# Kernel optimization log

Hardware: AMD Instinct MI355X
Metric: run time of the kernel (lower is better)

Reference implementation:

```python
import jax, jax.numpy as jnp
import numpy as np

N_NODES = 50000   # nodes per channel
N_EDGES = 800000  # intra edges per channel (avg degree ~16)
N_GRAPHS = 64     # graphs in the batch (global_add_pool segments)
D = 128           # node_features_len == out_channels
L = 3             # n_layers
BN_EPS = 1e-5
NEG_SLOPE = 0.01  # F.leaky_relu default


def setup_inputs() -> dict:
    key = jax.random.key(0)
    ks = jax.random.split(key, 24)
    s = 0.05
    inp = {
        "x1": jax.random.normal(ks[0], (N_NODES, D), jnp.float32),
        "x2": jax.random.normal(ks[1], (N_NODES, D), jnp.float32),
        # GIN MLP channel 1: Linear-BN-ReLU-Linear-ReLU, stacked over layers
        "W1_ch1": jax.random.normal(ks[2], (L, D, D), jnp.float32) * s,
        "b1_ch1": jax.random.normal(ks[3], (L, D), jnp.float32) * s,
        "bn_g": 1.0 + jax.random.normal(ks[4], (L, D), jnp.float32) * s,
        "bn_b": jax.random.normal(ks[5], (L, D), jnp.float32) * s,
        "bn_m": jax.random.normal(ks[6], (L, D), jnp.float32) * s,
        "bn_v": 0.5 + jax.random.uniform(ks[7], (L, D), jnp.float32),
        "W2_ch1": jax.random.normal(ks[8], (L, D, D), jnp.float32) * s,
        "b2_ch1": jax.random.normal(ks[9], (L, D), jnp.float32) * s,
        # GIN MLP channel 2: Linear-ReLU-Linear
        "W1_ch2": jax.random.normal(ks[10], (L, D, D), jnp.float32) * s,
        "b1_ch2": jax.random.normal(ks[11], (L, D), jnp.float32) * s,
        "W2_ch2": jax.random.normal(ks[12], (L, D, D), jnp.float32) * s,
        "b2_ch2": jax.random.normal(ks[13], (L, D), jnp.float32) * s,
        # head: Linear(2*D*L -> D) - ReLU - Dropout - Linear(D -> 1)
        "Wf1": jax.random.normal(ks[14], (2 * D * L, D), jnp.float32) * s,
        "bf1": jax.random.normal(ks[15], (D,), jnp.float32) * s,
        "Wf2": jax.random.normal(ks[16], (D, 1), jnp.float32) * s,
        "bf2": jax.random.normal(ks[17], (1,), jnp.float32) * s,
        "edge1": jax.random.randint(ks[18], (2, N_EDGES), 0, N_NODES, dtype=jnp.int32),
        "edge2": jax.random.randint(ks[19], (2, N_EDGES), 0, N_NODES, dtype=jnp.int32),
        "batch1": jnp.sort(jax.random.randint(ks[20], (N_NODES,), 0, N_GRAPHS, dtype=jnp.int32)),
        "batch2": jnp.sort(jax.random.randint(ks[21], (N_NODES,), 0, N_GRAPHS, dtype=jnp.int32)),
    }
    return inp


def _aggregate(x, edge):
    # GINConv sum aggregation: message x[src] scattered to dst; eps=0 default
    return jax.ops.segment_sum(x[edge[0]], edge[1], num_segments=N_NODES)


def _channel1(x, edge, batch, W1, b1, g, b, m, v, W2, b2):
    pooled = []
    for i in range(L):
        h = (x + _aggregate(x, edge)) @ W1[i] + b1[i]
        h = (h - m[i]) * (g[i] / jnp.sqrt(v[i] + BN_EPS)) + b[i]  # eval-mode BN
        h = jax.nn.relu(h)
        h = jax.nn.relu(h @ W2[i] + b2[i])
        x = jax.nn.leaky_relu(h, NEG_SLOPE)
        pooled.append(jax.ops.segment_sum(x, batch, num_segments=N_GRAPHS))
    return jnp.concatenate(pooled, axis=-1)  # [G, D*L]


def _channel2(x, edge, batch, W1, b1, W2, b2):
    pooled = []
    for i in range(L):
        h = jax.nn.relu((x + _aggregate(x, edge)) @ W1[i] + b1[i])
        h = h @ W2[i] + b2[i]
        x = jax.nn.leaky_relu(h, NEG_SLOPE)
        pooled.append(jax.ops.segment_sum(x, batch, num_segments=N_GRAPHS))
    return jnp.concatenate(pooled, axis=-1)  # [G, D*L]


def reference(x1, x2, W1_ch1, b1_ch1, bn_g, bn_b, bn_m, bn_v, W2_ch1, b2_ch1,
              W1_ch2, b1_ch2, W2_ch2, b2_ch2, Wf1, bf1, Wf2, bf2,
              edge1, edge2, batch1, batch2):
    p1 = _channel1(x1, edge1, batch1, W1_ch1, b1_ch1, bn_g, bn_b, bn_m, bn_v, W2_ch1, b2_ch1)
    p2 = _channel2(x2, edge2, batch2, W1_ch2, b1_ch2, W2_ch2, b2_ch2)
    z = jnp.concatenate([p1, p2], axis=-1)  # [G, 2*D*L]
    h = jax.nn.relu(z @ Wf1 + bf1)          # dropout is identity in eval mode
    return h @ Wf2 + bf2                    # [G, 1]
```

## Files before the change

### kernel.cpp

```cpp
#include <hip/hip_runtime.h>

#define NN 50000
#define NE 800000
#define TOTN (2 * NN)
#define NG 64
#define DD 128
#define NL 3
#define ZW (2 * DD * NL)
#define NB2 128
#define NPB 391
#define CAP2 8192
#define CHUNK 4096
#define P1B 196
#define GB2 1024

typedef __attribute__((ext_vector_type(8))) short short8;
typedef __attribute__((ext_vector_type(4))) float f32x4;

__device__ inline unsigned short f2bf(float f) {
  unsigned int u = __float_as_uint(f);
  unsigned int r = (u + 0x7fffu + ((u >> 16) & 1u)) >> 16;
  return (unsigned short)r;
}
__device__ inline float bflo(unsigned int u) { return __uint_as_float(u << 16); }
__device__ inline float bfhi(unsigned int u) { return __uint_as_float(u & 0xffff0000u); }

__global__ __launch_bounds__(256) void cvt_x_kernel(const float* __restrict__ x1,
                                                    const float* __restrict__ x2,
                                                    unsigned short* __restrict__ X) {
  int i = blockIdx.x * 256 + threadIdx.x;
  if (i >= TOTN * DD / 8) return;
  const int per = NN * DD / 8;
  int ch = i >= per;
  const float* x = ch ? x2 : x1;
  int il = i - ch * per;
  const float4* in4 = reinterpret_cast<const float4*>(x);
  float4 a = in4[2 * il], b = in4[2 * il + 1];
  uint4 o;
  o.x = (unsigned int)f2bf(a.x) | ((unsigned int)f2bf(a.y) << 16);
  o.y = (unsigned int)f2bf(a.z) | ((unsigned int)f2bf(a.w) << 16);
  o.z = (unsigned int)f2bf(b.x) | ((unsigned int)f2bf(b.y) << 16);
  o.w = (unsigned int)f2bf(b.z) | ((unsigned int)f2bf(b.w) << 16);
  reinterpret_cast<uint4*>(X)[i] = o;
}

__global__ __launch_bounds__(256) void cvt_wt_kernel(const float* __restrict__ p0,
                                                     const float* __restrict__ p1,
                                                     const float* __restrict__ p2,
                                                     const float* __restrict__ p3,
                                                     unsigned short* __restrict__ out) {
  __shared__ float tile[32][33];
  int slot = blockIdx.z;
  int grp = slot / 3, mat = slot % 3;
  const float* ip = (grp == 0 ? p0 : grp == 1 ? p1 : grp == 2 ? p2 : p3) + mat * 16384;
  unsigned short* op = out + slot * 16384;
  int k0 = blockIdx.x * 32, c0 = blockIdx.y * 32;
  int tx = threadIdx.x & 31, ty = threadIdx.x >> 5;
#pragma unroll
  for (int rr = 0; rr < 32; rr += 8)
    tile[ty + rr][tx] = ip[(k0 + ty + rr) * 128 + (c0 + tx)];
  __syncthreads();
#pragma unroll
  for (int rr = 0; rr < 32; rr += 8)
    op[(c0 + ty + rr) * 128 + (k0 + tx)] = f2bf(tile[tx][ty + rr]);
}

__global__ __launch_bounds__(256) void bucket_kernel(const int* __restrict__ e1,
                                                     const int* __restrict__ e2,
                                                     int* __restrict__ bcur,
                                                     uint2* __restrict__ pairs) {
  int ch = blockIdx.x >= P1B;
  int blk = blockIdx.x - ch * P1B;
  const int* E = ch ? e2 : e1;
  int base = blk * CHUNK;
  __shared__ int lcnt[NB2], gbase[NB2];
  for (int i = threadIdx.x; i < NB2; i += 256) lcnt[i] = 0;
  __syncthreads();
  int srcv[16], dstv[16], lrank[16];
#pragma unroll
  for (int k = 0; k < 16; k++) {
    int e = base + k * 256 + threadIdx.x;
    if (e < NE) {
      srcv[k] = E[e];
      dstv[k] = E[NE + e];
      lrank[k] = atomicAdd(&lcnt[dstv[k] / NPB], 1);
    } else dstv[k] = -1;
  }
  __syncthreads();
  for (int i = threadIdx.x; i < NB2; i += 256)
    gbase[i] = atomicAdd(&bcur[ch * NB2 + i], lcnt[i]);
  __syncthreads();
#pragma unroll
  for (int k = 0; k < 16; k++)
    if (dstv[k] >= 0) {
      int g = dstv[k] / NPB;
      pairs[(size_t)(ch * NB2 + g) * CAP2 + gbase[g] + lrank[k]] =
          make_uint2((unsigned)srcv[k], (unsigned)dstv[k]);
    }
}

__global__ __launch_bounds__(256) void scan_gstart_kernel(const int* __restrict__ bcur,
                                                          int* __restrict__ colbase,
                                                          const int* __restrict__ batch1,
                                                          const int* __restrict__ batch2,
                                                          int* __restrict__ gstart) {
  if (blockIdx.x == 0) {
    __shared__ int s[256];
    int tid = threadIdx.x;
    int v = bcur[tid];
    s[tid] = v;
    __syncthreads();
    int segstart = tid & ~127;
    for (int o = 1; o < 128; o <<= 1) {
      int t = (tid - o >= segstart) ? s[tid - o] : 0;
      __syncthreads();
      s[tid] += t;
      __syncthreads();
    }
    colbase[tid] = s[tid] - v;
  } else {
    int t = threadIdx.x;
    if (t >= 2 * (NG + 1)) return;
    int ch = t / (NG + 1), g = t % (NG + 1);
    const int* b = ch ? batch2 : batch1;
    int lo = 0, hi = NN;
    while (lo < hi) {
      int m = (lo + hi) >> 1;
      if (b[m] < g) lo = m + 1; else hi = m;
    }
    gstart[t] = lo;
  }
}

__global__ __launch_bounds__(256) void csr_build_kernel(const uint2* __restrict__ pairs,
                                                        const int* __restrict__ bcur,
                                                        const int* __restrict__ colbase,
                                                        int* __restrict__ rowptr,
                                                        int* __restrict__ col) {
  int g = blockIdx.x;
  int ch = g >> 7, b = g & 127;
  int node0 = b * NPB;
  int nloc = min(NPB, NN - node0);
  int count = bcur[g];
  int base = colbase[g];
  const uint2* p = pairs + (size_t)g * CAP2;
  __shared__ int hist[512], pref[512], cur[512], stmp[256];
  for (int i = threadIdx.x; i < 512; i += 256) hist[i] = 0;
  __syncthreads();
  for (int e = threadIdx.x; e < count; e += 256)
    atomicAdd(&hist[(int)p[e].y - node0], 1);
  __syncthreads();
  int t = threadIdx.x;
  int a0 = hist[2 * t], a1 = hist[2 * t + 1];
  int sum = a0 + a1;
  stmp[t] = sum;
  __syncthreads();
  for (int o = 1; o < 256; o <<= 1) {
    int tv = (t >= o) ? stmp[t - o] : 0;
    __syncthreads();
    stmp[t] += tv;
    __syncthreads();
  }
  int ex = stmp[t] - sum;
  pref[2 * t] = ex;       pref[2 * t + 1] = ex + a0;
  cur[2 * t] = ex;        cur[2 * t + 1] = ex + a0;
  __syncthreads();
  for (int i = threadIdx.x; i < nloc; i += 256)
    rowptr[ch * (NN + 1) + node0 + i] = base + pref[i];
  if (threadIdx.x == 0 && b == NB2 - 1) rowptr[ch * (NN + 1) + NN] = base + count;
  for (int e = threadIdx.x; e < count; e += 256) {
    uint2 pr = p[e];
    int pos = atomicAdd(&cur[(int)pr.y - node0], 1);
    col[ch * NE + base + pos] = (int)pr.x;
  }
}

__global__ __launch_bounds__(256, 4) void agg_kernel(const unsigned short* __restrict__ X,
                                                     const int* __restrict__ rowptr,
                                                     const int* __restrict__ col,
                                                     unsigned short* __restrict__ Y) {
  int node = blockIdx.x * 16 + (threadIdx.x >> 4);
  int lane = threadIdx.x & 15;
  int ch = node >= NN;
  int nl = node - ch * NN;
  const int* rp = rowptr + ch * (NN + 1);
  const int* cl = col + ch * NE;
  const uint4* X4 = reinterpret_cast<const uint4*>(X);
  size_t chbase = (size_t)ch * NN * 16;
  float acc[8];
  {
    uint4 sv = X4[(size_t)node * 16 + lane];
    unsigned int w[4] = {sv.x, sv.y, sv.z, sv.w};
#pragma unroll
    for (int q = 0; q < 4; q++) {
      acc[2 * q]     = bflo(w[q]);
      acc[2 * q + 1] = bfhi(w[q]);
    }
  }
  int s = rp[nl], e = rp[nl + 1];
  int j = s;
  for (; j + 16 <= e; j += 16) {
    int idx[16];
#pragma unroll
    for (int q = 0; q < 16; q++) idx[q] = cl[j + q];
    uint4 v[16];
#pragma unroll
    for (int q = 0; q < 16; q++) v[q] = X4[chbase + (size_t)idx[q] * 16 + lane];
#pragma unroll
    for (int q = 0; q < 16; q++) {
      unsigned int w[4] = {v[q].x, v[q].y, v[q].z, v[q].w};
#pragma unroll
      for (int u = 0; u < 4; u++) {
        acc[2 * u]     += bflo(w[u]);
        acc[2 * u + 1] += bfhi(w[u]);
      }
    }
  }
  for (; j + 4 <= e; j += 4) {
    int idx[4];
#pragma unroll
    for (int q = 0; q < 4; q++) idx[q] = cl[j + q];
    uint4 v[4];
#pragma unroll
    for (int q = 0; q < 4; q++) v[q] = X4[chbase + (size_t)idx[q] * 16 + lane];
#pragma unroll
    for (int q = 0; q < 4; q++) {
      unsigned int w[4] = {v[q].x, v[q].y, v[q].z, v[q].w};
#pragma unroll
      for (int u = 0; u < 4; u++) {
        acc[2 * u]     += bflo(w[u]);
        acc[2 * u + 1] += bfhi(w[u]);
      }
    }
  }
  for (; j < e; ++j) {
    uint4 v = X4[chbase + (size_t)cl[j] * 16 + lane];
    unsigned int w[4] = {v.x, v.y, v.z, v.w};
#pragma unroll
    for (int u = 0; u < 4; u++) {
      acc[2 * u]     += bflo(w[u]);
      acc[2 * u + 1] += bfhi(w[u]);
    }
  }
  uint4 o;
  unsigned int* ow = reinterpret_cast<unsigned int*>(&o);
#pragma unroll
  for (int q = 0; q < 4; q++)
    ow[q] = (unsigned int)f2bf(acc[2 * q]) | ((unsigned int)f2bf(acc[2 * q + 1]) << 16);
  reinterpret_cast<uint4*>(Y)[(size_t)node * 16 + lane] = o;
}

__global__ __launch_bounds__(256) void gemm_fused_kernel(
    const unsigned short* __restrict__ Y, unsigned short* __restrict__ X,
    const unsigned short* __restrict__ WT,
    const float* __restrict__ b1c1, const float* __restrict__ b1c2,
    const float* __restrict__ b2c1, const float* __restrict__ b2c2,
    const float* __restrict__ bng, const float* __restrict__ bnb,
    const float* __restrict__ bnm, const float* __restrict__ bnv, int layer) {
  __shared__ unsigned short hlds[16][136];
  int ch = blockIdx.x >= GB2;
  int lane = threadIdx.x & 63, wv = threadIdx.x >> 6;
  int l15 = lane & 15, lk = lane >> 4;
  int c0 = wv * 32;
  const unsigned short* W1 = WT + (size_t)(ch * 6 + layer) * 16384;
  const unsigned short* W2 = WT + (size_t)(ch * 6 + 3 + layer) * 16384;
  short8 w1f[2][4], w2f[2][4];
#pragma unroll
  for (int ct = 0; ct < 2; ct++)
#pragma unroll
    for (int kk = 0; kk < 4; kk++) {
      size_t boff = (size_t)(c0 + ct * 16 + l15) * 128 + kk * 32 + lk * 8;
      w1f[ct][kk] = *reinterpret_cast<const short8*>(W1 + boff);
      w2f[ct][kk] = *reinterpret_cast<const short8*>(W2 + boff);
    }
  const float* b1 = (ch ? b1c2 : b1c1) + layer * DD;
  const float* b2 = (ch ? b2c2 : b2c1) + layer * DD;
  float sc1[2], sh1[2], sh2[2];
#pragma unroll
  for (int ct = 0; ct < 2; ct++) {
    int colg = c0 + ct * 16 + l15;
    if (!ch) {
      float s = bng[layer * DD + colg] * rsqrtf(bnv[layer * DD + colg] + 1e-5f);
      sc1[ct] = s;
      sh1[ct] = (b1[colg] - bnm[layer * DD + colg]) * s + bnb[layer * DD + colg];
    } else {
      sc1[ct] = 1.f;
      sh1[ct] = b1[colg];
    }
    sh2[ct] = b2[colg];
  }
  int t0 = ch ? blockIdx.x - GB2 : blockIdx.x;
  short8 a0, a1, a2, a3;
  {
    size_t r0g = (size_t)ch * NN + t0 * 16;
    const unsigned short* yp = Y + (r0g + l15) * 128 + lk * 8;
    a0 = *reinterpret_cast<const short8*>(yp);
    a1 = *reinterpret_cast<const short8*>(yp + 32);
    a2 = *reinterpret_cast<const short8*>(yp + 64);
    a3 = *reinterpret_cast<const short8*>(yp + 96);
  }
  for (int t = t0; t < 3125; t += GB2) {
    int r0l = t * 16;
    size_t r0g = (size_t)ch * NN + r0l;
    short8 n0, n1, n2, n3;
    int tn = t + GB2;
    if (tn < 3125) {
      const unsigned short* yp = Y + ((size_t)ch * NN + tn * 16 + l15) * 128 + lk * 8;
      n0 = *reinterpret_cast<const short8*>(yp);
      n1 = *reinterpret_cast<const short8*>(yp + 32);
      n2 = *reinterpret_cast<const short8*>(yp + 64);
      n3 = *reinterpret_cast<const short8*>(yp + 96);
    }
#pragma unroll
    for (int ct = 0; ct < 2; ct++) {
      f32x4 acc = {0.f, 0.f, 0.f, 0.f};
      acc = __builtin_amdgcn_mfma_f32_16x16x32_bf16(a0, w1f[ct][0], acc, 0, 0, 0);
      acc = __builtin_amdgcn_mfma_f32_16x16x32_bf16(a1, w1f[ct][1], acc, 0, 0, 0);
      acc = __builtin_amdgcn_mfma_f32_16x16x32_bf16(a2, w1f[ct][2], acc, 0, 0, 0);
      acc = __builtin_amdgcn_mfma_f32_16x16x32_bf16(a3, w1f[ct][3], acc, 0, 0, 0);
      int colg = c0 + ct * 16 + l15;
#pragma unroll
      for (int r = 0; r < 4; r++) {
        float tv = fmaxf(acc[r] * sc1[ct] + sh1[ct], 0.f);
        hlds[lk * 4 + r][colg] = f2bf(tv);
      }
    }
    __syncthreads();
    short8 h0 = *reinterpret_cast<const short8*>(&hlds[l15][lk * 8]);
    short8 h1 = *reinterpret_cast<const short8*>(&hlds[l15][32 + lk * 8]);
    short8 h2 = *reinterpret_cast<const short8*>(&hlds[l15][64 + lk * 8]);
    short8 h3 = *reinterpret_cast<const short8*>(&hlds[l15][96 + lk * 8]);
#pragma unroll
    for (int ct = 0; ct < 2; ct++) {
      f32x4 acc = {0.f, 0.f, 0.f, 0.f};
      acc = __builtin_amdgcn_mfma_f32_16x16x32_bf16(h0, w2f[ct][0], acc, 0, 0, 0);
      acc = __builtin_amdgcn_mfma_f32_16x16x32_bf16(h1, w2f[ct][1], acc, 0, 0, 0);
      acc = __builtin_amdgcn_mfma_f32_16x16x32_bf16(h2, w2f[ct][2], acc, 0, 0, 0);
      acc = __builtin_amdgcn_mfma_f32_16x16x32_bf16(h3, w2f[ct][3], acc, 0, 0, 0);
      int colg = c0 + ct * 16 + l15;
#pragma unroll
      for (int r = 0; r < 4; r++) {
        float tv = acc[r] + sh2[ct];
        if (!ch) tv = fmaxf(tv, 0.f);
        else     tv = tv > 0.f ? tv : 0.01f * tv;
        X[(r0g + lk * 4 + r) * 128 + colg] = f2bf(tv);
      }
    }
    __syncthreads();
    a0 = n0; a1 = n1; a2 = n2; a3 = n3;
  }
}

__global__ __launch_bounds__(256) void pool_kernel(const unsigned short* __restrict__ X,
                                                   const int* __restrict__ gstart,
                                                   float* __restrict__ z, int layer) {
  int ch = blockIdx.x >> 6, g = blockIdx.x & 63;
  int r0 = gstart[ch * (NG + 1) + g], r1 = gstart[ch * (NG + 1) + g + 1];
  int c8 = threadIdx.x & 15, part = threadIdx.x >> 4;
  const uint4* X4 = reinterpret_cast<const uint4*>(X);
  size_t base = (size_t)ch * NN * 16 + c8;
  float acc[8];
#pragma unroll
  for (int q = 0; q < 8; q++) acc[q] = 0.f;
  int r = r0 + part;
  for (; r + 48 < r1; r += 64) {
    uint4 v0 = X4[base + (size_t)r * 16];
    uint4 v1 = X4[base + (size_t)(r + 16) * 16];
    uint4 v2 = X4[base + (size_t)(r + 32) * 16];
    uint4 v3 = X4[base + (size_t)(r + 48) * 16];
    unsigned int w0[4] = {v0.x, v0.y, v0.z, v0.w};
    unsigned int w1[4] = {v1.x, v1.y, v1.z, v1.w};
    unsigned int w2[4] = {v2.x, v2.y, v2.z, v2.w};
    unsigned int w3[4] = {v3.x, v3.y, v3.z, v3.w};
#pragma unroll
    for (int q = 0; q < 4; q++) {
      acc[2 * q]     += bflo(w0[q]) + bflo(w1[q]) + bflo(w2[q]) + bflo(w3[q]);
      acc[2 * q + 1] += bfhi(w0[q]) + bfhi(w1[q]) + bfhi(w2[q]) + bfhi(w3[q]);
    }
  }
  for (; r < r1; r += 16) {
    uint4 v = X4[base + (size_t)r * 16];
    unsigned int w[4] = {v.x, v.y, v.z, v.w};
#pragma unroll
    for (int q = 0; q < 4; q++) {
      acc[2 * q]     += bflo(w[q]);
      acc[2 * q + 1] += bfhi(w[q]);
    }
  }
  __shared__ float zacc[16][128];
#pragma unroll
  for (int q = 0; q < 8; q++) zacc[part][c8 * 8 + q] = acc[q];
  __syncthreads();
  for (int s = 8; s > 0; s >>= 1) {
    if (part < s) {
#pragma unroll
      for (int q = 0; q < 8; q++)
        zacc[part][c8 * 8 + q] += zacc[part + s][c8 * 8 + q];
    }
    __syncthreads();
  }
  if (part == 0) {
#pragma unroll
    for (int q = 0; q < 8; q++) {
      int colw = c8 * 8 + q;
      z[(size_t)g * ZW + ch * DD * NL + layer * DD + colw] = zacc[0][colw];
    }
  }
}

__global__ __launch_bounds__(128) void head_kernel(const float* __restrict__ z,
                                                   const float* __restrict__ Wf1,
                                                   const float* __restrict__ bf1,
                                                   const float* __restrict__ Wf2,
                                                   const float* __restrict__ bf2,
                                                   float* __restrict__ out) {
  int g = blockIdx.x, t = threadIdx.x;
  const float* zr = z + (size_t)g * ZW;
  float acc = bf1[t];
  for (int j = 0; j < ZW; ++j) acc += zr[j] * Wf1[(size_t)j * DD + t];
  float h = fmaxf(acc, 0.f);
  __shared__ float red[128];
  red[t] = h * Wf2[t];
  __syncthreads();
  for (int s = 64; s > 0; s >>= 1) {
    if (t < s) red[t] += red[t + s];
    __syncthreads();
  }
  if (t == 0) out[g] = red[0] + bf2[0];
}

extern "C" void kernel_launch(void* const* d_in, const int* in_sizes, int n_in,
                              void* d_out, int out_size, void* d_ws, size_t ws_size,
                              hipStream_t stream) {
  const float* x1   = (const float*)d_in[0];
  const float* x2   = (const float*)d_in[1];
  const float* W1c1 = (const float*)d_in[2];
  const float* b1c1 = (const float*)d_in[3];
  const float* bng  = (const float*)d_in[4];
  const float* bnb  = (const float*)d_in[5];
  const float* bnm  = (const float*)d_in[6];
  const float* bnv  = (const float*)d_in[7];
  const float* W2c1 = (const float*)d_in[8];
  const float* b2c1 = (const float*)d_in[9];
  const float* W1c2 = (const float*)d_in[10];
  const float* b1c2 = (const float*)d_in[11];
  const float* W2c2 = (const float*)d_in[12];
  const float* b2c2 = (const float*)d_in[13];
  const float* Wf1  = (const float*)d_in[14];
  const float* bf1  = (const float*)d_in[15];
  const float* Wf2  = (const float*)d_in[16];
  const float* bf2  = (const float*)d_in[17];
  const int* edge1  = (const int*)d_in[18];
  const int* edge2  = (const int*)d_in[19];
  const int* batch1 = (const int*)d_in[20];
  const int* batch2 = (const int*)d_in[21];
  (void)ws_size; (void)n_in; (void)in_sizes; (void)out_size;

  char* ws = (char*)d_ws;
  const size_t NB16 = (size_t)TOTN * DD * 2;
  unsigned short* bufA = (unsigned short*)(ws);
  unsigned short* bufB = (unsigned short*)(ws + NB16);
  unsigned short* bufY = (unsigned short*)(ws + 2 * NB16);
  size_t off = 3 * NB16;
  unsigned short* WT = (unsigned short*)(ws + off); off += (size_t)12 * 16384 * 2;
  uint2* pairs = (uint2*)(ws + off); off += (size_t)2 * NB2 * CAP2 * 8;
  int* col     = (int*)(ws + off); off += (size_t)2 * NE * 4;
  int* rowptr  = (int*)(ws + off); off += (((size_t)2 * (NN + 1) * 4) + 255) & ~(size_t)255;
  int* bcur    = (int*)(ws + off); off += 256 * 4;
  int* colbase = (int*)(ws + off); off += 256 * 4;
  int* gstart  = (int*)(ws + off); off += 256 * 4;
  float* z     = (float*)(ws + off); off += (size_t)NG * ZW * 4;

  cvt_wt_kernel<<<dim3(4, 4, 12), 256, 0, stream>>>(W1c1, W2c1, W1c2, W2c2, WT);
  hipMemsetAsync(bcur, 0, 256 * 4, stream);
  cvt_x_kernel<<<(TOTN * DD / 8 + 255) / 256, 256, 0, stream>>>(x1, x2, bufA);

  bucket_kernel<<<2 * P1B, 256, 0, stream>>>(edge1, edge2, bcur, pairs);
  scan_gstart_kernel<<<2, 256, 0, stream>>>(bcur, colbase, batch1, batch2, gstart);
  csr_build_kernel<<<2 * NB2, 256, 0, stream>>>(pairs, bcur, colbase, rowptr, col);

  unsigned short* cin = bufA;
  unsigned short* cout = bufB;
  for (int i = 0; i < NL; ++i) {
    agg_kernel<<<TOTN / 16, 256, 0, stream>>>(cin, rowptr, col, bufY);
    gemm_fused_kernel<<<2 * GB2, 256, 0, stream>>>(bufY, cout, WT,
                                                   b1c1, b1c2, b2c1, b2c2,
                                                   bng, bnb, bnm, bnv, i);
    pool_kernel<<<2 * NG, 256, 0, stream>>>(cout, gstart, z, i);
    unsigned short* tmp = cin; cin = cout; cout = tmp;
  }

  head_kernel<<<NG, 128, 0, stream>>>(z, Wf1, bf1, Wf2, bf2, (float*)d_out);
}
```

Before: 390.2 us.

## Merge prep kernels and fold pooling into next layer's aggregation launch

Combines the bf16 input conversion, weight transpose and edge bucketing into one prep kernel launch. Each layer's segment-sum pooling now runs as extra blocks inside the following layer's aggregation kernel, reading the same layer output, with one standalone pool launch kept for the last layer. The gather loop drops from 16-wide to 8-wide unrolling and loses the occupancy hint in launch bounds. This cuts kernel launches and serial gaps between small kernels, at the cost of pool blocks competing with aggregation blocks and less memory-level parallelism in the gather.

```diff
diff --git a/kernel.cpp b/kernel.cpp
--- a/kernel.cpp
+++ b/kernel.cpp
@@ -13,6 +13,8 @@
 #define CHUNK 4096
 #define P1B 196
 #define GB2 1024
+#define AGGB (TOTN / 16)
+#define CVTX (TOTN * DD / 8 / 256)
 
 typedef __attribute__((ext_vector_type(8))) short short8;
 typedef __attribute__((ext_vector_type(4))) float f32x4;
@@ -25,78 +27,79 @@
 __device__ inline float bflo(unsigned int u) { return __uint_as_float(u << 16); }
 __device__ inline float bfhi(unsigned int u) { return __uint_as_float(u & 0xffff0000u); }
 
-__global__ __launch_bounds__(256) void cvt_x_kernel(const float* __restrict__ x1,
-                                                    const float* __restrict__ x2,
-                                                    unsigned short* __restrict__ X) {
-  int i = blockIdx.x * 256 + threadIdx.x;
-  if (i >= TOTN * DD / 8) return;
-  const int per = NN * DD / 8;
-  int ch = i >= per;
-  const float* x = ch ? x2 : x1;
-  int il = i - ch * per;
-  const float4* in4 = reinterpret_cast<const float4*>(x);
-  float4 a = in4[2 * il], b = in4[2 * il + 1];
-  uint4 o;
-  o.x = (unsigned int)f2bf(a.x) | ((unsigned int)f2bf(a.y) << 16);
-  o.y = (unsigned int)f2bf(a.z) | ((unsigned int)f2bf(a.w) << 16);
-  o.z = (unsigned int)f2bf(b.x) | ((unsigned int)f2bf(b.y) << 16);
-  o.w = (unsigned int)f2bf(b.z) | ((unsigned int)f2bf(b.w) << 16);
-  reinterpret_cast<uint4*>(X)[i] = o;
-}
-
-__global__ __launch_bounds__(256) void cvt_wt_kernel(const float* __restrict__ p0,
-                                                     const float* __restrict__ p1,
-                                                     const float* __restrict__ p2,
-                                                     const float* __restrict__ p3,
-                                                     unsigned short* __restrict__ out) {
-  __shared__ float tile[32][33];
-  int slot = blockIdx.z;
-  int grp = slot / 3, mat = slot % 3;
-  const float* ip = (grp == 0 ? p0 : grp == 1 ? p1 : grp == 2 ? p2 : p3) + mat * 16384;
-  unsigned short* op = out + slot * 16384;
-  int k0 = blockIdx.x * 32, c0 = blockIdx.y * 32;
-  int tx = threadIdx.x & 31, ty = threadIdx.x >> 5;
-#pragma unroll
-  for (int rr = 0; rr < 32; rr += 8)
-    tile[ty + rr][tx] = ip[(k0 + ty + rr) * 128 + (c0 + tx)];
-  __syncthreads();
-#pragma unroll
-  for (int rr = 0; rr < 32; rr += 8)
-    op[(c0 + ty + rr) * 128 + (k0 + tx)] = f2bf(tile[tx][ty + rr]);
-}
-
-__global__ __launch_bounds__(256) void bucket_kernel(const int* __restrict__ e1,
-                                                     const int* __restrict__ e2,
-                                                     int* __restrict__ bcur,
-                                                     uint2* __restrict__ pairs) {
-  int ch = blockIdx.x >= P1B;
-  int blk = blockIdx.x - ch * P1B;
-  const int* E = ch ? e2 : e1;
-  int base = blk * CHUNK;
-  __shared__ int lcnt[NB2], gbase[NB2];
-  for (int i = threadIdx.x; i < NB2; i += 256) lcnt[i] = 0;
-  __syncthreads();
-  int srcv[16], dstv[16], lrank[16];
-#pragma unroll
-  for (int k = 0; k < 16; k++) {
-    int e = base + k * 256 + threadIdx.x;
-    if (e < NE) {
-      srcv[k] = E[e];
-      dstv[k] = E[NE + e];
-      lrank[k] = atomicAdd(&lcnt[dstv[k] / NPB], 1);
-    } else dstv[k] = -1;
-  }
-  __syncthreads();
-  for (int i = threadIdx.x; i < NB2; i += 256)
-    gbase[i] = atomicAdd(&bcur[ch * NB2 + i], lcnt[i]);
-  __syncthreads();
-#pragma unroll
-  for (int k = 0; k < 16; k++)
-    if (dstv[k] >= 0) {
-      int g = dstv[k] / NPB;
-      pairs[(size_t)(ch * NB2 + g) * CAP2 + gbase[g] + lrank[k]] =
-          make_uint2((unsigned)srcv[k], (unsigned)dstv[k]);
-    }
+__global__ __launch_bounds__(256) void prep_kernel(
+    const float* __restrict__ x1, const float* __restrict__ x2,
+    unsigned short* __restrict__ X,
+    const float* __restrict__ p0, const float* __restrict__ p1,
+    const float* __restrict__ p2, const float* __restrict__ p3,
+    unsigned short* __restrict__ WT,
+    const int* __restrict__ e1, const int* __restrict__ e2,
+    int* __restrict__ bcur, uint2* __restrict__ pairs) {
+  int bid = blockIdx.x;
+  if (bid < CVTX) {
+    int i = bid * 256 + threadIdx.x;
+    const int per = NN * DD / 8;
+    int ch = i >= per;
+    const float* x = ch ? x2 : x1;
+    int il = i - ch * per;
+    const float4* in4 = reinterpret_cast<const float4*>(x);
+    float4 a = in4[2 * il], b = in4[2 * il + 1];
+    uint4 o;
+    o.x = (unsigned int)f2bf(a.x) | ((unsigned int)f2bf(a.y) << 16);
+    o.y = (unsigned int)f2bf(a.z) | ((unsigned int)f2bf(a.w) << 16);
+    o.z = (unsigned int)f2bf(b.x) | ((unsigned int)f2bf(b.y) << 16);
+    o.w = (unsigned int)f2bf(b.z) | ((unsigned int)f2bf(b.w) << 16);
+    reinterpret_cast<uint4*>(X)[i] = o;
+    return;
+  }
+  if (bid < CVTX + 192) {
+    __shared__ float tile[32][33];
+    int idx = bid - CVTX;
+    int k0 = (idx & 3) * 32, c0 = ((idx >> 2) & 3) * 32, slot = idx >> 4;
+    int grp = slot / 3, mat = slot % 3;
+    const float* ip = (grp == 0 ? p0 : grp == 1 ? p1 : grp == 2 ? p2 : p3) + mat * 16384;
+    unsigned short* op = WT + slot * 16384;
+    int tx = threadIdx.x & 31, ty = threadIdx.x >> 5;
+#pragma unroll
+    for (int rr = 0; rr < 32; rr += 8)
+      tile[ty + rr][tx] = ip[(k0 + ty + rr) * 128 + (c0 + tx)];
+    __syncthreads();
+#pragma unroll
+    for (int rr = 0; rr < 32; rr += 8)
+      op[(c0 + ty + rr) * 128 + (k0 + tx)] = f2bf(tile[tx][ty + rr]);
+    return;
+  }
+  {
+    int blk = bid - (CVTX + 192);
+    int ch = blk >= P1B;
+    blk -= ch * P1B;
+    const int* E = ch ? e2 : e1;
+    int base = blk * CHUNK;
+    __shared__ int lcnt[NB2], gbase[NB2];
+    for (int i = threadIdx.x; i < NB2; i += 256) lcnt[i] = 0;
+    __syncthreads();
+    int srcv[16], dstv[16], lrank[16];
+#pragma unroll
+    for (int k = 0; k < 16; k++) {
+      int e = base + k * 256 + threadIdx.x;
+      if (e < NE) {
+        srcv[k] = E[e];
+        dstv[k] = E[NE + e];
+        lrank[k] = atomicAdd(&lcnt[dstv[k] / NPB], 1);
+      } else dstv[k] = -1;
+    }
+    __syncthreads();
+    for (int i = threadIdx.x; i < NB2; i += 256)
+      gbase[i] = atomicAdd(&bcur[ch * NB2 + i], lcnt[i]);
+    __syncthreads();
+#pragma unroll
+    for (int k = 0; k < 16; k++)
+      if (dstv[k] >= 0) {
+        int g = dstv[k] / NPB;
+        pairs[(size_t)(ch * NB2 + g) * CAP2 + gbase[g] + lrank[k]] =
+            make_uint2((unsigned)srcv[k], (unsigned)dstv[k]);
+      }
+  }
 }
 
 __global__ __launch_bounds__(256) void scan_gstart_kernel(const int* __restrict__ bcur,
@@ -175,10 +178,69 @@
   }
 }
 
-__global__ __launch_bounds__(256, 4) void agg_kernel(const unsigned short* __restrict__ X,
-                                                     const int* __restrict__ rowptr,
-                                                     const int* __restrict__ col,
-                                                     unsigned short* __restrict__ Y) {
+__global__ __launch_bounds__(256) void agg_pool_kernel(const unsigned short* __restrict__ X,
+                                                       const int* __restrict__ rowptr,
+                                                       const int* __restrict__ col,
+                                                       unsigned short* __restrict__ Y,
+                                                       const unsigned short* __restrict__ Xprev,
+                                                       const int* __restrict__ gstart,
+                                                       float* __restrict__ z, int layerPrev) {
+  if (blockIdx.x >= AGGB) {
+    int pb = blockIdx.x - AGGB;
+    int ch = pb >> 6, g = pb & 63;
+    int r0 = gstart[ch * (NG + 1) + g], r1 = gstart[ch * (NG + 1) + g + 1];
+    int c8 = threadIdx.x & 15, part = threadIdx.x >> 4;
+    const uint4* X4 = reinterpret_cast<const uint4*>(Xprev);
+    size_t base = (size_t)ch * NN * 16 + c8;
+    float acc[8];
+#pragma unroll
+    for (int q = 0; q < 8; q++) acc[q] = 0.f;
+    int r = r0 + part;
+    for (; r + 48 < r1; r += 64) {
+      uint4 v0 = X4[base + (size_t)r * 16];
+      uint4 v1 = X4[base + (size_t)(r + 16) * 16];
+      uint4 v2 = X4[base + (size_t)(r + 32) * 16];
+      uint4 v3 = X4[base + (size_t)(r + 48) * 16];
+      unsigned int w0[4] = {v0.x, v0.y, v0.z, v0.w};
+      unsigned int w1[4] = {v1.x, v1.y, v1.z, v1.w};
+      unsigned int w2[4] = {v2.x, v2.y, v2.z, v2.w};
+      unsigned int w3[4] = {v3.x, v3.y, v3.z, v3.w};
+#pragma unroll
+      for (int q = 0; q < 4; q++) {
+        acc[2 * q]     += bflo(w0[q]) + bflo(w1[q]) + bflo(w2[q]) + bflo(w3[q]);
+        acc[2 * q + 1] += bfhi(w0[q]) + bfhi(w1[q]) + bfhi(w2[q]) + bfhi(w3[q]);
+      }
+    }
+    for (; r < r1; r += 16) {
+      uint4 v = X4[base + (size_t)r * 16];
+      unsigned int w[4] = {v.x, v.y, v.z, v.w};
+#pragma unroll
+      for (int q = 0; q < 4; q++) {
+        acc[2 * q]     += bflo(w[q]);
+        acc[2 * q + 1] += bfhi(w[q]);
+      }
+    }
+    __shared__ float zacc[16][128];
+#pragma unroll
+    for (int q = 0; q < 8; q++) zacc[part][c8 * 8 + q] = acc[q];
+    __syncthreads();
+    for (int s = 8; s > 0; s >>= 1) {
+      if (part < s) {
+#pragma unroll
+        for (int q = 0; q < 8; q++)
+          zacc[part][c8 * 8 + q] += zacc[part + s][c8 * 8 + q];
+      }
+      __syncthreads();
+    }
+    if (part == 0) {
+#pragma unroll
+      for (int q = 0; q < 8; q++) {
+        int colw = c8 * 8 + q;
+        z[(size_t)g * ZW + ch * DD * NL + layerPrev * DD + colw] = zacc[0][colw];
+      }
+    }
+    return;
+  }
   int node = blockIdx.x * 16 + (threadIdx.x >> 4);
   int lane = threadIdx.x & 15;
   int ch = node >= NN;
@@ -199,32 +261,13 @@
   }
   int s = rp[nl], e = rp[nl + 1];
   int j = s;
-  for (; j + 16 <= e; j += 16) {
-    int idx[16];
-#pragma unroll
-    for (int q = 0; q < 16; q++) idx[q] = cl[j + q];
-    uint4 v[16];
-#pragma unroll
-    for (int q = 0; q < 16; q++) v[q] = X4[chbase + (size_t)idx[q] * 16 + lane];
-#pragma unroll
-    for (int q = 0; q < 16; q++) {
-      unsigned int w[4] = {v[q].x, v[q].y, v[q].z, v[q].w};
-#pragma unroll
-      for (int u = 0; u < 4; u++) {
-        acc[2 * u]     += bflo(w[u]);
-        acc[2 * u + 1] += bfhi(w[u]);
-      }
-    }
-  }
-  for (; j + 4 <= e; j += 4) {
-    int idx[4];
-#pragma unroll
-    for (int q = 0; q < 4; q++) idx[q] = cl[j + q];
-    uint4 v[4];
-#pragma unroll
-    for (int q = 0; q < 4; q++) v[q] = X4[chbase + (size_t)idx[q] * 16 + lane];
-#pragma unroll
-    for (int q = 0; q < 4; q++) {
+  for (; j + 8 <= e; j += 8) {
+    uint4 v[8];
+#pragma unroll
+    for (int q = 0; q < 8; q++)
+      v[q] = X4[chbase + (size_t)cl[j + q] * 16 + lane];
+#pragma unroll
+    for (int q = 0; q < 8; q++) {
       unsigned int w[4] = {v[q].x, v[q].y, v[q].z, v[q].w};
 #pragma unroll
       for (int u = 0; u < 4; u++) {
@@ -471,24 +514,23 @@
   int* gstart  = (int*)(ws + off); off += 256 * 4;
   float* z     = (float*)(ws + off); off += (size_t)NG * ZW * 4;
 
-  cvt_wt_kernel<<<dim3(4, 4, 12), 256, 0, stream>>>(W1c1, W2c1, W1c2, W2c2, WT);
   hipMemsetAsync(bcur, 0, 256 * 4, stream);
-  cvt_x_kernel<<<(TOTN * DD / 8 + 255) / 256, 256, 0, stream>>>(x1, x2, bufA);
-
-  bucket_kernel<<<2 * P1B, 256, 0, stream>>>(edge1, edge2, bcur, pairs);
+  prep_kernel<<<CVTX + 192 + 2 * P1B, 256, 0, stream>>>(
+      x1, x2, bufA, W1c1, W2c1, W1c2, W2c2, WT, edge1, edge2, bcur, pairs);
   scan_gstart_kernel<<<2, 256, 0, stream>>>(bcur, colbase, batch1, batch2, gstart);
   csr_build_kernel<<<2 * NB2, 256, 0, stream>>>(pairs, bcur, colbase, rowptr, col);
 
   unsigned short* cin = bufA;
   unsigned short* cout = bufB;
   for (int i = 0; i < NL; ++i) {
-    agg_kernel<<<TOTN / 16, 256, 0, stream>>>(cin, rowptr, col, bufY);
+    int grid = (i == 0) ? AGGB : AGGB + 2 * NG;
+    agg_pool_kernel<<<grid, 256, 0, stream>>>(cin, rowptr, col, bufY,
+                                              cin, gstart, z, i - 1);
     gemm_fused_kernel<<<2 * GB2, 256, 0, stream>>>(bufY, cout, WT,
                                                    b1c1, b1c2, b2c1, b2c2,
                                                    bng, bnb, bnm, bnv, i);
-    pool_kernel<<<2 * NG, 256, 0, stream>>>(cout, gstart, z, i);
     unsigned short* tmp = cin; cin = cout; cout = tmp;
   }
-
+  pool_kernel<<<2 * NG, 256, 0, stream>>>(cin, gstart, z, NL - 1);
   head_kernel<<<NG, 128, 0, stream>>>(z, Wf1, bf1, Wf2, bf2, (float*)d_out);
 }
```

New measurement: 375.9 us. 1.04x faster.
